# Optimization experiments

Measured on AMD Instinct MI355X. Metric: run time of the kernel, lower is better.

## Reference

```python
import jax, jax.numpy as jnp
import numpy as np

D_MODEL = 1024
H = 16
DH = 64
FFN = 4096
CHUNK = 64
LN_EPS = 1e-5


def layer_norm(x, w, b):
    mu = x.mean(-1, keepdims=True)
    var = x.var(-1, keepdims=True)
    return (x - mu) * jax.lax.rsqrt(var + LN_EPS) * w + b


def l2_normalize(x):
    # matches torch F.normalize(p=2, dim=-1, eps=1e-12)
    n = jnp.sqrt(jnp.sum(x * x, axis=-1, keepdims=True))
    return x / jnp.maximum(n, 1e-12)


def chunk_gla(q, k, v, alpha, C=CHUNK):
    B, Hh, N, D = q.shape
    nc = N // C  # N chosen as multiple of C (pad==0 in original)
    q = q.reshape(B, Hh, nc, C, D)
    k = k.reshape(B, Hh, nc, C, D)
    v = v.reshape(B, Hh, nc, C, D)
    alpha = alpha.reshape(B, Hh, nc, C, D)

    log_a = jnp.log(jnp.maximum(alpha, 1e-6))
    la_cum = jnp.cumsum(log_a, axis=3)                  # (B,H,nc,C,D)
    la_mean = la_cum.mean(-1)                            # (B,H,nc,C)
    tril = jnp.tril(jnp.ones((C, C), dtype=q.dtype))
    decay = jnp.exp(la_mean[..., :, None] - la_mean[..., None, :]) * tril  # (B,H,nc,C,C)

    attn_intra = jnp.einsum('bhncd,bhnmd->bhncm', q, k) * decay
    o_intra = jnp.einsum('bhncm,bhnmd->bhncd', attn_intra, v)

    decay_to_end = jnp.exp(la_cum[:, :, :, -1:, :] - la_cum)
    kv_chunk = jnp.einsum('bhncf,bhnce->bhnfe', k * decay_to_end, v)  # (B,H,nc,D,D)
    chunk_decay = jnp.exp(log_a.sum(3))                  # (B,H,nc,D)
    q_dec = q * jnp.exp(la_cum)                          # decay_from_start

    def step(S, inp):
        qd, kv, cd = inp                                 # (B,H,C,D),(B,H,D,D),(B,H,D)
        o = jnp.einsum('bhcd,bhde->bhce', qd, S)
        S_new = S * cd[:, :, :, None] + kv
        return S_new, o

    S0 = jnp.zeros((B, Hh, D, D), dtype=q.dtype)
    _, o_inter = jax.lax.scan(
        step, S0,
        (jnp.moveaxis(q_dec, 2, 0), jnp.moveaxis(kv_chunk, 2, 0), jnp.moveaxis(chunk_decay, 2, 0)))
    o_inter = jnp.moveaxis(o_inter, 0, 2)                # (B,H,nc,C,D)
    return (o_intra + o_inter).reshape(B, Hh, N, D)


def setup_inputs() -> dict:
    key = jax.random.key(0)
    ks = jax.random.split(key, 16)
    s = 0.02
    td = H * DH
    return {
        'x': jax.random.normal(ks[0], (2, 4096, D_MODEL), dtype=jnp.float32),
        'Wq': jax.random.normal(ks[1], (D_MODEL, td), dtype=jnp.float32) * s,
        'Wk': jax.random.normal(ks[2], (D_MODEL, td), dtype=jnp.float32) * s,
        'Wv': jax.random.normal(ks[3], (D_MODEL, td), dtype=jnp.float32) * s,
        'Wg': jax.random.normal(ks[4], (D_MODEL, td), dtype=jnp.float32) * s,
        'bg': jnp.full((td,), -0.5, dtype=jnp.float32),
        'Wo': jax.random.normal(ks[5], (td, D_MODEL), dtype=jnp.float32) * s,
        'ln1_w': jnp.ones((D_MODEL,), jnp.float32),
        'ln1_b': jnp.zeros((D_MODEL,), jnp.float32),
        'ln2_w': jnp.ones((D_MODEL,), jnp.float32),
        'ln2_b': jnp.zeros((D_MODEL,), jnp.float32),
        'W1': jax.random.normal(ks[6], (D_MODEL, FFN), dtype=jnp.float32) * s,
        'b1': jnp.zeros((FFN,), jnp.float32),
        'W2': jax.random.normal(ks[7], (FFN, D_MODEL), dtype=jnp.float32) * s,
        'b2': jnp.zeros((D_MODEL,), jnp.float32),
    }


def reference(x, Wq, Wk, Wv, Wg, bg, Wo, ln1_w, ln1_b, ln2_w, ln2_b, W1, b1, W2, b2):
    B, N, _ = x.shape
    xn = layer_norm(x, ln1_w, ln1_b)
    q = (xn @ Wq).reshape(B, N, H, DH).transpose(0, 2, 1, 3)
    k = (xn @ Wk).reshape(B, N, H, DH).transpose(0, 2, 1, 3)
    v = (xn @ Wv).reshape(B, N, H, DH).transpose(0, 2, 1, 3)
    q = l2_normalize(q)
    k = l2_normalize(k)
    alpha = jax.nn.sigmoid(xn @ Wg + bg).reshape(B, N, H, DH).transpose(0, 2, 1, 3)
    o = chunk_gla(q, k, v, alpha)
    o = o.transpose(0, 2, 1, 3).reshape(B, N, H * DH)
    x = x + o @ Wo  # dropout off (eval / p=0)
    h = layer_norm(x, ln2_w, ln2_b)
    x = x + jax.nn.gelu(h @ W1 + b1, approximate=False) @ W2 + b2
    return x
```

## Files before the change

kernel.cpp:

```cpp
#include <hip/hip_runtime.h>

#define AS1 __attribute__((address_space(1)))
#define AS3 __attribute__((address_space(3)))

typedef unsigned short u16;
typedef short s16x8 __attribute__((ext_vector_type(8)));
typedef float f32x4 __attribute__((ext_vector_type(4)));
typedef float f32x16 __attribute__((ext_vector_type(16)));

__device__ __forceinline__ float bf2f(u16 u) {
    union { unsigned u; float f; } v; v.u = ((unsigned)u) << 16; return v.f;
}
__device__ __forceinline__ u16 f2bf(float f) {
    union { float f; unsigned u; } v; v.f = f;
    unsigned u = v.u;
    return (u16)((u + 0x7FFFu + ((u >> 16) & 1u)) >> 16);
}

__device__ __forceinline__ void gload16(const void* g, void* l) {
    __builtin_amdgcn_global_load_lds((const AS1 void*)g, (AS3 void*)l, 16, 0, 0);
}

__global__ __launch_bounds__(256) void transpose_bf16(
    const float* __restrict__ src, u16* __restrict__ dst, int R, int C)
{
    __shared__ float t[32][33];
    const int tx = threadIdx.x, ty = threadIdx.y;
    const int r0 = blockIdx.x * 32, c0 = blockIdx.y * 32;
#pragma unroll
    for (int i = 0; i < 4; i++)
        t[ty + i * 8][tx] = src[(size_t)(r0 + ty + i * 8) * C + c0 + tx];
    __syncthreads();
#pragma unroll
    for (int i = 0; i < 4; i++)
        dst[(size_t)(c0 + ty + i * 8) * R + r0 + tx] = f2bf(t[tx][ty + i * 8]);
}

__global__ __launch_bounds__(256) void ln_bf16(
    const float* __restrict__ x, const float* __restrict__ w,
    const float* __restrict__ b, u16* __restrict__ out)
{
    __shared__ float red[8];
    const int row = blockIdx.x;
    const int tid = threadIdx.x;
    const size_t base = (size_t)row * 1024 + tid * 4;
    const float4 xv = *(const float4*)&x[base];
    float s = xv.x + xv.y + xv.z + xv.w;
    float q = xv.x * xv.x + xv.y * xv.y + xv.z * xv.z + xv.w * xv.w;
#pragma unroll
    for (int m = 1; m < 64; m <<= 1) { s += __shfl_xor(s, m); q += __shfl_xor(q, m); }
    if ((tid & 63) == 0) { red[tid >> 6] = s; red[4 + (tid >> 6)] = q; }
    __syncthreads();
    s = red[0] + red[1] + red[2] + red[3];
    q = red[4] + red[5] + red[6] + red[7];
    const float mu = s * (1.f / 1024.f);
    const float var = q * (1.f / 1024.f) - mu * mu;
    const float rs = rsqrtf(var + 1e-5f);
    const float4 wv = *(const float4*)&w[tid * 4];
    const float4 bv = *(const float4*)&b[tid * 4];
    uint2 ov;
    ov.x = (unsigned)f2bf((xv.x - mu) * rs * wv.x + bv.x) |
           ((unsigned)f2bf((xv.y - mu) * rs * wv.y + bv.y) << 16);
    ov.y = (unsigned)f2bf((xv.z - mu) * rs * wv.z + bv.z) |
           ((unsigned)f2bf((xv.w - mu) * rs * wv.w + bv.w) << 16);
    *(uint2*)&out[base] = ov;
}

template <int EPX>
__global__ __launch_bounds__(256, 2) void gemm32(
    const u16* __restrict__ A, const u16* __restrict__ BT,
    float* __restrict__ Cf, u16* __restrict__ Cb,
    const float* __restrict__ bias, const float* __restrict__ resid,
    int M, int N, int K)
{
    __shared__ u16 As[2][8192];
    __shared__ u16 Bs[2][8192];
    const int tid = threadIdx.x;
    const int w = tid >> 6, l = tid & 63;
    const int tm = blockIdx.x * 128, tn = blockIdx.y * 128;
    const int wm = (w >> 1) * 64, wn = (w & 1) * 64;

    const int srow = l >> 3;
    const int scol = ((l & 7) ^ srow) * 8;
    size_t aSb[4], bSb[4];
#pragma unroll
    for (int j = 0; j < 4; j++) {
        aSb[j] = (size_t)(tm + w * 32 + j * 8 + srow) * K + scol;
        bSb[j] = (size_t)(tn + w * 32 + j * 8 + srow) * K + scol;
    }

    auto stage = [&](int t, int buf) {
        const int k0 = t * 64;
#pragma unroll
        for (int j = 0; j < 4; j++)
            gload16(&A[aSb[j] + k0], &As[buf][(w * 32 + j * 8) * 64]);
#pragma unroll
        for (int j = 0; j < 4; j++)
            gload16(&BT[bSb[j] + k0], &Bs[buf][(w * 32 + j * 8) * 64]);
    };

    int aoff[2][4], boff[2][4];
#pragma unroll
    for (int mm = 0; mm < 2; mm++)
#pragma unroll
        for (int ks = 0; ks < 4; ks++) {
            const int g = ((ks * 2 + (l >> 5)) ^ (l & 7)) * 8;
            aoff[mm][ks] = (wm + mm * 32 + (l & 31)) * 64 + g;
            boff[mm][ks] = (wn + mm * 32 + (l & 31)) * 64 + g;
        }

    f32x16 acc[2][2] = {};

    stage(0, 0);
    stage(1, 1);
    asm volatile("s_waitcnt vmcnt(8)" ::: "memory");
    __builtin_amdgcn_s_barrier();

    const int NT = K >> 6;
    for (int t = 0; t < NT; ++t) {
        const int buf = t & 1;
        const u16* as = As[buf];
        const u16* bs = Bs[buf];
        s16x8 a0[2][2], b0[2][2], a1[2][2], b1[2][2];
#pragma unroll
        for (int ks = 0; ks < 2; ks++)
#pragma unroll
            for (int mm = 0; mm < 2; mm++) {
                a0[mm][ks] = *(const s16x8*)&as[aoff[mm][ks]];
                b0[mm][ks] = *(const s16x8*)&bs[boff[mm][ks]];
            }
        __builtin_amdgcn_s_setprio(1);
#pragma unroll
        for (int ks = 0; ks < 2; ks++)
#pragma unroll
            for (int mm = 0; mm < 2; mm++)
#pragma unroll
                for (int nn = 0; nn < 2; nn++)
                    acc[mm][nn] = __builtin_amdgcn_mfma_f32_32x32x16_bf16(
                        a0[mm][ks], b0[nn][ks], acc[mm][nn], 0, 0, 0);
        __builtin_amdgcn_s_setprio(0);
#pragma unroll
        for (int ks = 0; ks < 2; ks++)
#pragma unroll
            for (int mm = 0; mm < 2; mm++) {
                a1[mm][ks] = *(const s16x8*)&as[aoff[mm][ks + 2]];
                b1[mm][ks] = *(const s16x8*)&bs[boff[mm][ks + 2]];
            }
        asm volatile("s_waitcnt lgkmcnt(0)" ::: "memory");
        __builtin_amdgcn_sched_barrier(0);
        __builtin_amdgcn_s_barrier();
        const bool st = (t + 2 < NT);
        if (st) stage(t + 2, buf);
        __builtin_amdgcn_s_setprio(1);
#pragma unroll
        for (int ks = 0; ks < 2; ks++)
#pragma unroll
            for (int mm = 0; mm < 2; mm++)
#pragma unroll
                for (int nn = 0; nn < 2; nn++)
                    acc[mm][nn] = __builtin_amdgcn_mfma_f32_32x32x16_bf16(
                        a1[mm][ks], b1[nn][ks], acc[mm][nn], 0, 0, 0);
        __builtin_amdgcn_s_setprio(0);
        if (st)              asm volatile("s_waitcnt vmcnt(8)" ::: "memory");
        else if (t + 1 < NT) asm volatile("s_waitcnt vmcnt(0)" ::: "memory");
        __builtin_amdgcn_s_barrier();
    }

#pragma unroll
    for (int mm = 0; mm < 2; mm++)
#pragma unroll
        for (int nn = 0; nn < 2; nn++)
#pragma unroll
            for (int reg = 0; reg < 16; reg++) {
                const int row = tm + wm + mm * 32 + (l >> 5) * 4 + (reg & 3) + (reg >> 2) * 8;
                const int col = tn + wn + nn * 32 + (l & 31);
                const float v = acc[mm][nn][reg];
                if (EPX == 0) {
                    if (col < 3072) Cb[(size_t)row * 3072 + col] = f2bf(v);
                    else            Cf[(size_t)row * 1024 + (col - 3072)] = v;
                } else if (EPX == 1) {
                    const float u2 = v + bias[col];
                    Cb[(size_t)row * N + col] =
                        f2bf(0.5f * u2 * (1.f + erff(u2 * 0.70710678118654752f)));
                } else if (EPX == 2) {
                    const size_t idx = (size_t)row * N + col;
                    Cf[idx] = v + resid[idx];
                } else {
                    const size_t idx = (size_t)row * N + col;
                    Cf[idx] = v + bias[col] + resid[idx];
                }
            }
}

#define TP 72
#define LP 65
__global__ __launch_bounds__(256) void gla_a(
    const u16* __restrict__ qkv,
    const float* __restrict__ g,
    const float* __restrict__ bg,
    u16* __restrict__ qdec,
    u16* __restrict__ kvT,
    float* __restrict__ cdec,
    u16* __restrict__ ointra)
{
    __shared__ u16 Qh[64 * TP];
    __shared__ u16 Kh[64 * TP];
    __shared__ u16 VT[64 * TP];
    __shared__ float L[64 * LP];
    __shared__ float lm[64], nq[64], nk[64];

    const int bid = blockIdx.x;
    const int bh = bid >> 6, ck = bid & 63;
    const int b = bh >> 4, h = bh & 15;
    const int tok0 = b * 4096 + ck * 64;
    const int tid = threadIdx.x;
    const int w = tid >> 6, l = tid & 63;

#pragma unroll
    for (int pass = 0; pass < 2; pass++) {
        const int c = (tid >> 3) + pass * 32;
        const int col = (tid & 7) * 8;
        const size_t rb = (size_t)(tok0 + c) * 3072 + h * 64 + col;
        uint4 qv = *(const uint4*)&qkv[rb];
        uint4 kv_ = *(const uint4*)&qkv[rb + 1024];
        uint4 vv = *(const uint4*)&qkv[rb + 2048];
        *(uint4*)&Qh[c * TP + col] = qv;
        *(uint4*)&Kh[c * TP + col] = kv_;
        const u16* va = (const u16*)&vv;
#pragma unroll
        for (int j = 0; j < 8; j++) VT[(col + j) * TP + c] = va[j];
    }
#pragma unroll
    for (int pass = 0; pass < 4; pass++) {
        const int c = (tid >> 4) + pass * 16;
        const int col = (tid & 15) * 4;
        float4 gv = *(const float4*)&g[(size_t)(tok0 + c) * 1024 + h * 64 + col];
        float4 bgv = *(const float4*)&bg[h * 64 + col];
        const float* ga = (const float*)&gv;
        const float* ba = (const float*)&bgv;
#pragma unroll
        for (int i = 0; i < 4; i++) {
            const float z = ga[i] + ba[i];
            const float al = 1.f / (1.f + __expf(-z));
            L[c * LP + col + i] = __logf(fmaxf(al, 1e-6f));
        }
    }
    __syncthreads();

    {
        const int d = tid >> 2, qq = tid & 3;
        float vals[16];
#pragma unroll
        for (int i = 0; i < 16; i++) vals[i] = L[(qq * 16 + i) * LP + d];
        float s = 0.f;
#pragma unroll
        for (int i = 0; i < 16; i++) { s += vals[i]; vals[i] = s; }
        float sum = s;
        float u1 = __shfl_up(sum, 1, 4); if (qq >= 1) sum += u1;
        float u2 = __shfl_up(sum, 2, 4); if (qq >= 2) sum += u2;
        const float excl = sum - s;
#pragma unroll
        for (int i = 0; i < 16; i++) L[(qq * 16 + i) * LP + d] = vals[i] + excl;
        if (qq == 3) cdec[((size_t)bh * 64 + ck) * 64 + d] = __expf(sum);
    }
    __syncthreads();

    {
        const int c = tid >> 2, qq = tid & 3;
        float sl = 0.f, sq = 0.f, sk = 0.f;
        uint4 qa = *(const uint4*)&Qh[c * TP + qq * 16];
        uint4 qb = *(const uint4*)&Qh[c * TP + qq * 16 + 8];
        uint4 ka = *(const uint4*)&Kh[c * TP + qq * 16];
        uint4 kb = *(const uint4*)&Kh[c * TP + qq * 16 + 8];
        const u16* qu = (const u16*)&qa; const u16* qu2 = (const u16*)&qb;
        const u16* ku = (const u16*)&ka; const u16* ku2 = (const u16*)&kb;
#pragma unroll
        for (int i = 0; i < 8; i++) {
            float q1 = bf2f(qu[i]), q2 = bf2f(qu2[i]);
            float k1 = bf2f(ku[i]), k2 = bf2f(ku2[i]);
            sq += q1 * q1 + q2 * q2;
            sk += k1 * k1 + k2 * k2;
        }
#pragma unroll
        for (int i = 0; i < 16; i++) sl += L[c * LP + qq * 16 + i];
        sl += __shfl_xor(sl, 1); sl += __shfl_xor(sl, 2);
        sq += __shfl_xor(sq, 1); sq += __shfl_xor(sq, 2);
        sk += __shfl_xor(sk, 1); sk += __shfl_xor(sk, 2);
        if (qq == 0) {
            lm[c] = sl * (1.f / 64.f);
            nq[c] = 1.f / fmaxf(sqrtf(sq), 1e-12f);
            nk[c] = 1.f / fmaxf(sqrtf(sk), 1e-12f);
        }
    }
    __syncthreads();

    u16 kdt[16];
    {
        const int c = tid >> 2, qq = tid & 3;
        const float qn = nq[c], kn = nk[c];
        uint4 qa = *(const uint4*)&Qh[c * TP + qq * 16];
        uint4 qb = *(const uint4*)&Qh[c * TP + qq * 16 + 8];
        uint4 ka = *(const uint4*)&Kh[c * TP + qq * 16];
        uint4 kb = *(const uint4*)&Kh[c * TP + qq * 16 + 8];
        u16* qu = (u16*)&qa; u16* qu2 = (u16*)&qb;
        u16* ku = (u16*)&ka; u16* ku2 = (u16*)&kb;
        float Lc[16], Le[16];
#pragma unroll
        for (int i = 0; i < 16; i++) {
            Lc[i] = L[c * LP + qq * 16 + i];
            Le[i] = L[63 * LP + qq * 16 + i];
        }
        unsigned pk[8];
#pragma unroll
        for (int i = 0; i < 8; i++) {
            float qh1 = bf2f(qu[i]) * qn;  qu[i] = f2bf(qh1);
            float qh2 = bf2f(qu2[i]) * qn; qu2[i] = f2bf(qh2);
            float kh1 = bf2f(ku[i]) * kn;  ku[i] = f2bf(kh1);
            float kh2 = bf2f(ku2[i]) * kn; ku2[i] = f2bf(kh2);
            kdt[i]     = f2bf(kh1 * __expf(Le[i] - Lc[i]));
            kdt[i + 8] = f2bf(kh2 * __expf(Le[i + 8] - Lc[i + 8]));
        }
#pragma unroll
        for (int i = 0; i < 4; i++) {
            pk[i] = (unsigned)f2bf(bf2f(qu[2 * i]) * __expf(Lc[2 * i])) |
                    ((unsigned)f2bf(bf2f(qu[2 * i + 1]) * __expf(Lc[2 * i + 1])) << 16);
            pk[4 + i] = (unsigned)f2bf(bf2f(qu2[2 * i]) * __expf(Lc[8 + 2 * i])) |
                        ((unsigned)f2bf(bf2f(qu2[2 * i + 1]) * __expf(Lc[8 + 2 * i + 1])) << 16);
        }
        *(uint4*)&Qh[c * TP + qq * 16] = qa;
        *(uint4*)&Qh[c * TP + qq * 16 + 8] = qb;
        *(uint4*)&Kh[c * TP + qq * 16] = ka;
        *(uint4*)&Kh[c * TP + qq * 16 + 8] = kb;
        u16* qrow = &qdec[((size_t)bh * 4096 + ck * 64 + c) * 64 + qq * 16];
        *(uint4*)&qrow[0] = *(const uint4*)&pk[0];
        *(uint4*)&qrow[8] = *(const uint4*)&pk[4];
    }
    __syncthreads();

    u16* KDT = (u16*)L;
    {
        const int c = tid >> 2, qq = tid & 3;
#pragma unroll
        for (int i = 0; i < 16; i++) KDT[(qq * 16 + i) * TP + c] = kdt[i];
    }
    const int fr = l & 15;
    const int kk = (l >> 4) * 8;
    f32x4 accS[4] = {};
#pragma unroll
    for (int ks = 0; ks < 2; ks++) {
        s16x8 af = *(const s16x8*)&Qh[(w * 16 + fr) * TP + ks * 32 + kk];
#pragma unroll
        for (int j = 0; j < 4; j++) {
            s16x8 bf = *(const s16x8*)&Kh[(j * 16 + fr) * TP + ks * 32 + kk];
            accS[j] = __builtin_amdgcn_mfma_f32_16x16x32_bf16(af, bf, accS[j], 0, 0, 0);
        }
    }
    __syncthreads();

    {
        const int erow = w * 16 + (l >> 4) * 4;
#pragma unroll
        for (int j = 0; j < 4; j++) {
            const int mm = j * 16 + (l & 15);
            const float lmm = lm[mm];
#pragma unroll
            for (int r = 0; r < 4; r++) {
                const int cc = erow + r;
                const float wgt = (mm <= cc) ? __expf(lm[cc] - lmm) : 0.f;
                Qh[cc * TP + mm] = f2bf(accS[j][r] * wgt);
            }
        }
    }
    __syncthreads();

    f32x4 accO[4] = {};
    f32x4 accK[4] = {};
#pragma unroll
    for (int ks = 0; ks < 2; ks++) {
        s16x8 aAt = *(const s16x8*)&Qh[(w * 16 + fr) * TP + ks * 32 + kk];
        s16x8 aVt = *(const s16x8*)&VT[(w * 16 + fr) * TP + ks * 32 + kk];
#pragma unroll
        for (int j = 0; j < 4; j++) {
            s16x8 bVt = *(const s16x8*)&VT[(j * 16 + fr) * TP + ks * 32 + kk];
            s16x8 bKd = *(const s16x8*)&KDT[(j * 16 + fr) * TP + ks * 32 + kk];
            accO[j] = __builtin_amdgcn_mfma_f32_16x16x32_bf16(aAt, bVt, accO[j], 0, 0, 0);
            accK[j] = __builtin_amdgcn_mfma_f32_16x16x32_bf16(aVt, bKd, accK[j], 0, 0, 0);
        }
    }
    {
        const int erow = w * 16 + (l >> 4) * 4;
#pragma unroll
        for (int j = 0; j < 4; j++) {
            const int col = j * 16 + (l & 15);
#pragma unroll
            for (int r = 0; r < 4; r++) {
                const int row = erow + r;
                ointra[((size_t)bh * 4096 + ck * 64 + row) * 64 + col] = f2bf(accO[j][r]);
                kvT[(((size_t)bh * 64 + ck) * 64 + row) * 64 + col] = f2bf(accK[j][r]);
            }
        }
    }
}

__global__ __launch_bounds__(256) void gla_scan(
    const u16* __restrict__ kvT, const float* __restrict__ cdec,
    u16* __restrict__ ST)
{
    const int bh = blockIdx.x >> 4;
    const int de = (blockIdx.x & 15) * 256 + threadIdx.x;
    const int d = de & 63;
    float s = 0.f;
    const size_t base = (size_t)bh * 64 * 4096 + de;
    const size_t cb = (size_t)bh * 4096 + d;
    for (int t = 0; t < 64; t++) {
        ST[base + (size_t)t * 4096] = f2bf(s);
        s = s * cdec[cb + (size_t)t * 64] + bf2f(kvT[base + (size_t)t * 4096]);
    }
}

__global__ __launch_bounds__(256) void gla_b(
    const u16* __restrict__ qdec, const u16* __restrict__ ST,
    const u16* __restrict__ ointra, u16* __restrict__ obf)
{
    __shared__ u16 Qd[64 * TP];
    __shared__ u16 Sd[64 * TP];
    const int bid = blockIdx.x;
    const int bh = bid >> 6, ck = bid & 63;
    const int b = bh >> 4, h = bh & 15;
    const int tid = threadIdx.x;
    const int w = tid >> 6, l = tid & 63;
#pragma unroll
    for (int pass = 0; pass < 2; pass++) {
        const int r = (tid >> 3) + pass * 32;
        const int col = (tid & 7) * 8;
        *(uint4*)&Qd[r * TP + col] =
            *(const uint4*)&qdec[((size_t)bh * 4096 + ck * 64 + r) * 64 + col];
        *(uint4*)&Sd[r * TP + col] =
            *(const uint4*)&ST[(((size_t)bh * 64 + ck) * 64 + r) * 64 + col];
    }
    __syncthreads();
    const int fr = l & 15;
    const int kk = (l >> 4) * 8;
    f32x4 acc[4] = {};
#pragma unroll
    for (int ks = 0; ks < 2; ks++) {
        s16x8 af = *(const s16x8*)&Qd[(w * 16 + fr) * TP + ks * 32 + kk];
#pragma unroll
        for (int j = 0; j < 4; j++) {
            s16x8 bf = *(const s16x8*)&Sd[(j * 16 + fr) * TP + ks * 32 + kk];
            acc[j] = __builtin_amdgcn_mfma_f32_16x16x32_bf16(af, bf, acc[j], 0, 0, 0);
        }
    }
    const int erow = w * 16 + (l >> 4) * 4;
#pragma unroll
    for (int j = 0; j < 4; j++) {
        const int e = j * 16 + (l & 15);
#pragma unroll
        for (int r = 0; r < 4; r++) {
            const int cc = erow + r;
            const size_t ia = ((size_t)bh * 4096 + ck * 64 + cc) * 64 + e;
            const float v = acc[j][r] + bf2f(ointra[ia]);
            obf[(size_t)(b * 4096 + ck * 64 + cc) * 1024 + h * 64 + e] = f2bf(v);
        }
    }
}

__global__ void fill_sentinel(float* out, int n) {
    int i = blockIdx.x * 256 + threadIdx.x;
    if (i < n) out[i] = 12345.0f;
}

extern "C" void kernel_launch(void* const* d_in, const int* in_sizes, int n_in,
                              void* d_out, int out_size, void* d_ws, size_t ws_size,
                              hipStream_t stream)
{
    const float* x    = (const float*)d_in[0];
    const float* Wq   = (const float*)d_in[1];
    const float* Wk   = (const float*)d_in[2];
    const float* Wv   = (const float*)d_in[3];
    const float* Wg   = (const float*)d_in[4];
    const float* bg   = (const float*)d_in[5];
    const float* Wo   = (const float*)d_in[6];
    const float* ln1w = (const float*)d_in[7];
    const float* ln1b = (const float*)d_in[8];
    const float* ln2w = (const float*)d_in[9];
    const float* ln2b = (const float*)d_in[10];
    const float* W1   = (const float*)d_in[11];
    const float* b1   = (const float*)d_in[12];
    const float* W2   = (const float*)d_in[13];
    const float* b2   = (const float*)d_in[14];
    float* out = (float*)d_out;

    char* ws = (char*)d_ws;
    u16*   wtQKVG = (u16*)(ws + 0);
    u16*   wtWo   = (u16*)(ws + 8388608);
    u16*   wtW1   = (u16*)(ws + 10485760);
    u16*   wtW2   = (u16*)(ws + 18874368);
    u16*   xnb    = (u16*)(ws + 27262976);
    u16*   qkvb   = (u16*)(ws + 44040192);
    float* gbuf   = (float*)(ws + 94371840);
    u16*   kvT    = (u16*)(ws + 127926272);
    float* cdbuf  = (float*)(ws + 144703488);
    u16*   qdecb  = (u16*)(ws + 145227776);
    u16*   ointra = (u16*)(ws + 162004992);
    u16*   STb    = (u16*)(ws + 178782208);
    u16*   obf    = (u16*)(ws + 195559424);
    u16*   hbf    = (u16*)(ws + 212336640);
    float* x2     = (float*)(ws + 94371840);
    u16*   ffnb   = (u16*)(ws + 27262976);

    if (ws_size < 229113856u) {
        fill_sentinel<<<dim3((out_size + 255) / 256), dim3(256), 0, stream>>>(out, out_size);
        return;
    }

    const dim3 b256(256), b32x8(32, 8);

    transpose_bf16<<<dim3(32, 32),  b32x8, 0, stream>>>(Wq, wtQKVG,               1024, 1024);
    transpose_bf16<<<dim3(32, 32),  b32x8, 0, stream>>>(Wk, wtQKVG + 1024 * 1024, 1024, 1024);
    transpose_bf16<<<dim3(32, 32),  b32x8, 0, stream>>>(Wv, wtQKVG + 2048 * 1024, 1024, 1024);
    transpose_bf16<<<dim3(32, 32),  b32x8, 0, stream>>>(Wg, wtQKVG + 3072 * 1024, 1024, 1024);
    transpose_bf16<<<dim3(32, 32),  b32x8, 0, stream>>>(Wo, wtWo,                 1024, 1024);
    transpose_bf16<<<dim3(32, 128), b32x8, 0, stream>>>(W1, wtW1,                 1024, 4096);
    transpose_bf16<<<dim3(128, 32), b32x8, 0, stream>>>(W2, wtW2,                 4096, 1024);

    ln_bf16<<<dim3(8192), b256, 0, stream>>>(x, ln1w, ln1b, xnb);
    gemm32<0><<<dim3(64, 32), b256, 0, stream>>>(xnb, wtQKVG, gbuf, qkvb, nullptr, nullptr, 8192, 4096, 1024);

    gla_a<<<dim3(2048), b256, 0, stream>>>(qkvb, gbuf, bg, qdecb, kvT, cdbuf, ointra);
    gla_scan<<<dim3(512), b256, 0, stream>>>(kvT, cdbuf, STb);
    gla_b<<<dim3(2048), b256, 0, stream>>>(qdecb, STb, ointra, obf);

    gemm32<2><<<dim3(64, 8), b256, 0, stream>>>(obf, wtWo, x2, nullptr, nullptr, x, 8192, 1024, 1024);
    ln_bf16<<<dim3(8192), b256, 0, stream>>>(x2, ln2w, ln2b, hbf);
    gemm32<1><<<dim3(64, 32), b256, 0, stream>>>(hbf, wtW1, nullptr, ffnb, b1, nullptr, 8192, 4096, 1024);
    gemm32<4><<<dim3(64, 8), b256, 0, stream>>>(ffnb, wtW2, out, nullptr, b2, x2, 8192, 1024, 4096);
}
```

Baseline: 425.0 us.

## Halve GEMM K-tile to 32 and raise occupancy to four blocks per CU

The bf16 MFMA GEMM now stages K-slices of 32 instead of 64, which halves the LDS footprint per block (32KB to 16KB). It raises launch bounds to allow four resident blocks per CU. The LDS swizzle, the load offsets and the vmcnt waits are reworked for the narrower tile, and the loop drops its two-phase split. This trades twice as many barriers and loop iterations, with less MFMA work between them, for more waves available to hide memory latency, and register pressure rises under the tighter launch bound.

```diff
diff --git a/kernel.cpp b/kernel.cpp
--- a/kernel.cpp
+++ b/kernel.cpp
@@ -67,84 +67,70 @@
 }
 
 template <int EPX>
-__global__ __launch_bounds__(256, 2) void gemm32(
+__global__ __launch_bounds__(256, 4) void gemm32(
     const u16* __restrict__ A, const u16* __restrict__ BT,
     float* __restrict__ Cf, u16* __restrict__ Cb,
     const float* __restrict__ bias, const float* __restrict__ resid,
     int M, int N, int K)
 {
-    __shared__ u16 As[2][8192];
-    __shared__ u16 Bs[2][8192];
+    __shared__ u16 As[2][4096];
+    __shared__ u16 Bs[2][4096];
     const int tid = threadIdx.x;
     const int w = tid >> 6, l = tid & 63;
     const int tm = blockIdx.x * 128, tn = blockIdx.y * 128;
     const int wm = (w >> 1) * 64, wn = (w & 1) * 64;
 
-    const int srow = l >> 3;
-    const int scol = ((l & 7) ^ srow) * 8;
-    size_t aSb[4], bSb[4];
-#pragma unroll
-    for (int j = 0; j < 4; j++) {
-        aSb[j] = (size_t)(tm + w * 32 + j * 8 + srow) * K + scol;
-        bSb[j] = (size_t)(tn + w * 32 + j * 8 + srow) * K + scol;
+    const int srow = l >> 2;
+    const int sg = ((l & 3) ^ ((l >> 3) & 3)) * 8;
+    size_t aSb[2], bSb[2];
+#pragma unroll
+    for (int j = 0; j < 2; j++) {
+        aSb[j] = (size_t)(tm + w * 32 + j * 16 + srow) * K + sg;
+        bSb[j] = (size_t)(tn + w * 32 + j * 16 + srow) * K + sg;
     }
 
     auto stage = [&](int t, int buf) {
-        const int k0 = t * 64;
-#pragma unroll
-        for (int j = 0; j < 4; j++)
-            gload16(&A[aSb[j] + k0], &As[buf][(w * 32 + j * 8) * 64]);
-#pragma unroll
-        for (int j = 0; j < 4; j++)
-            gload16(&BT[bSb[j] + k0], &Bs[buf][(w * 32 + j * 8) * 64]);
+        const int k0 = t * 32;
+#pragma unroll
+        for (int j = 0; j < 2; j++)
+            gload16(&A[aSb[j] + k0], &As[buf][(w * 32 + j * 16) * 32]);
+#pragma unroll
+        for (int j = 0; j < 2; j++)
+            gload16(&BT[bSb[j] + k0], &Bs[buf][(w * 32 + j * 16) * 32]);
     };
 
-    int aoff[2][4], boff[2][4];
+    const int hi = l >> 5;
+    int aoff[2][2], boff[2][2];
 #pragma unroll
     for (int mm = 0; mm < 2; mm++)
 #pragma unroll
-        for (int ks = 0; ks < 4; ks++) {
-            const int g = ((ks * 2 + (l >> 5)) ^ (l & 7)) * 8;
-            aoff[mm][ks] = (wm + mm * 32 + (l & 31)) * 64 + g;
-            boff[mm][ks] = (wn + mm * 32 + (l & 31)) * 64 + g;
+        for (int ks = 0; ks < 2; ks++) {
+            const int ra = wm + mm * 32 + (l & 31);
+            const int rb = wn + mm * 32 + (l & 31);
+            const int key = ((l & 31) >> 1) & 3;
+            aoff[mm][ks] = ra * 32 + ((ks * 2 + hi) ^ key) * 8;
+            boff[mm][ks] = rb * 32 + ((ks * 2 + hi) ^ key) * 8;
         }
 
     f32x16 acc[2][2] = {};
 
     stage(0, 0);
     stage(1, 1);
-    asm volatile("s_waitcnt vmcnt(8)" ::: "memory");
+    asm volatile("s_waitcnt vmcnt(4)" ::: "memory");
     __builtin_amdgcn_s_barrier();
 
-    const int NT = K >> 6;
+    const int NT = K >> 5;
     for (int t = 0; t < NT; ++t) {
         const int buf = t & 1;
         const u16* as = As[buf];
         const u16* bs = Bs[buf];
-        s16x8 a0[2][2], b0[2][2], a1[2][2], b1[2][2];
-#pragma unroll
-        for (int ks = 0; ks < 2; ks++)
-#pragma unroll
-            for (int mm = 0; mm < 2; mm++) {
-                a0[mm][ks] = *(const s16x8*)&as[aoff[mm][ks]];
-                b0[mm][ks] = *(const s16x8*)&bs[boff[mm][ks]];
-            }
-        __builtin_amdgcn_s_setprio(1);
-#pragma unroll
-        for (int ks = 0; ks < 2; ks++)
-#pragma unroll
-            for (int mm = 0; mm < 2; mm++)
-#pragma unroll
-                for (int nn = 0; nn < 2; nn++)
-                    acc[mm][nn] = __builtin_amdgcn_mfma_f32_32x32x16_bf16(
-                        a0[mm][ks], b0[nn][ks], acc[mm][nn], 0, 0, 0);
-        __builtin_amdgcn_s_setprio(0);
-#pragma unroll
-        for (int ks = 0; ks < 2; ks++)
-#pragma unroll
-            for (int mm = 0; mm < 2; mm++) {
-                a1[mm][ks] = *(const s16x8*)&as[aoff[mm][ks + 2]];
-                b1[mm][ks] = *(const s16x8*)&bs[boff[mm][ks + 2]];
+        s16x8 a[2][2], b[2][2];
+#pragma unroll
+        for (int mm = 0; mm < 2; mm++)
+#pragma unroll
+            for (int ks = 0; ks < 2; ks++) {
+                a[mm][ks] = *(const s16x8*)&as[aoff[mm][ks]];
+                b[mm][ks] = *(const s16x8*)&bs[boff[mm][ks]];
             }
         asm volatile("s_waitcnt lgkmcnt(0)" ::: "memory");
         __builtin_amdgcn_sched_barrier(0);
@@ -159,9 +145,9 @@
 #pragma unroll
                 for (int nn = 0; nn < 2; nn++)
                     acc[mm][nn] = __builtin_amdgcn_mfma_f32_32x32x16_bf16(
-                        a1[mm][ks], b1[nn][ks], acc[mm][nn], 0, 0, 0);
+                        a[mm][ks], b[nn][ks], acc[mm][nn], 0, 0, 0);
         __builtin_amdgcn_s_setprio(0);
-        if (st)              asm volatile("s_waitcnt vmcnt(8)" ::: "memory");
+        if (st)              asm volatile("s_waitcnt vmcnt(4)" ::: "memory");
         else if (t + 1 < NT) asm volatile("s_waitcnt vmcnt(0)" ::: "memory");
         __builtin_amdgcn_s_barrier();
     }
```

Result: no change. 423.2 us (-0.4%).
